# Kernel optimization log

Measured on AMD Instinct MI355X. Metric: run time of the kernel, lower is better.

The kernel has to match this reference:

```python
import jax, jax.numpy as jnp
import numpy as np

WIN = 15
BINS = 32
ALPHA = 0.9
LAM1 = 0.5
LAM2 = 0.5


def _tmedian(x, axis):
    # torch-style median: k-th smallest with k=(n-1)//2 (lower middle), keepdims
    n = x.shape[axis]
    s = jnp.sort(x, axis=axis)
    return jnp.take(s, jnp.array([(n - 1) // 2]), axis=axis)


def _box_sum_1d(x, k, axis):
    # sliding-window sum (zero padding) via cumsum / integral image
    p = k // 2
    L = x.shape[axis]
    c = jnp.cumsum(x, axis=axis)
    pad = [(0, 0)] * x.ndim
    pad[axis] = (1, 0)
    c = jnp.pad(c, pad)
    i = jnp.arange(L)
    hi = jnp.clip(i + p + 1, 0, L)
    lo = jnp.clip(i - p, 0, L)
    return jnp.take(c, hi, axis=axis) - jnp.take(c, lo, axis=axis)


def _counts_1d(L, k, dtype):
    p = k // 2
    i = jnp.arange(L)
    return (jnp.clip(i + p + 1, 0, L) - jnp.clip(i - p, 0, L)).astype(dtype)


def box_avg(x, k):
    # avg_pool2d(stride=1, padding=k//2, count_include_pad=False) on [B,C,H,W]
    s = _box_sum_1d(_box_sum_1d(x, k, 2), k, 3)
    c = _counts_1d(x.shape[2], k, x.dtype)[:, None] * _counts_1d(x.shape[3], k, x.dtype)[None, :]
    return s / c


def avg3(x):
    # avg_pool2d(k=3, stride=1, pad=1, count_include_pad=True)
    return _box_sum_1d(_box_sum_1d(x, 3, 2), 3, 3) / 9.0


def _softplus(x):
    t = jnp.log1p(jnp.exp(-jnp.abs(x)))
    return jnp.where(x >= 0, x + t, t)


def _conv3(x, k):
    return jax.lax.conv_general_dilated(x, k, (1, 1), ((1, 1), (1, 1)),
                                        dimension_numbers=('NCHW', 'OIHW', 'NCHW'))


def _forward(lab, a_rand):
    B, _, H, W = lab.shape
    N = H * W
    f32 = lab.dtype
    L = lab[:, 0:1]
    a = lab[:, 1:2]
    b = lab[:, 2:3]
    kx = jnp.array([[-1, 0, 1], [-2, 0, 2], [-1, 0, 1]], f32).reshape(1, 1, 3, 3)
    ky = jnp.array([[-1, -2, -1], [0, 0, 0], [1, 2, 1]], f32).reshape(1, 1, 3, 3)
    gx = _conv3(L, kx)
    gy = _conv3(L, ky)
    E = avg3(gx * gx) + avg3(gy * gy)           # structure-tensor trace
    S = jnp.sqrt(a * a + b * b + 1e-8)           # chroma
    Xf = jnp.concatenate([E, S], 1).reshape(B, 2, N).transpose(0, 2, 1)   # [B,N,2]
    yf = L.reshape(B, 1, N).transpose(0, 2, 1)                            # [B,N,1]
    XtX = jnp.einsum('bni,bnj->bij', Xf, Xf)
    XtY = jnp.einsum('bni,bnj->bij', Xf, yf)
    beta = jnp.linalg.solve(XtX + 1e-6 * jnp.eye(2, dtype=f32), XtY)[..., 0]  # [B,2]
    pred = beta[:, 0][:, None, None, None] * E + beta[:, 1][:, None, None, None] * S
    L_perp = L - pred
    # robust scale + whitening of [L_perp, E, S]
    X3f = jnp.concatenate([L_perp, E, S], 1).reshape(B, 3, N).transpose(0, 2, 1)  # [B,N,3]
    med = _tmedian(X3f, 1)
    mad = _tmedian(jnp.abs(X3f - med), 1) * 1.4826 + 1e-8
    Xz = (X3f - med) / mad
    diff = Xz - Xz.mean(1, keepdims=True)
    cov = jnp.einsum('bni,bnj->bij', diff, diff) / N
    e, V = jnp.linalg.eigh(jnp.maximum(cov, 1e-8))
    Wwh = jnp.einsum('bij,bj,bkj->bik', V, 1.0 / jnp.sqrt(e), V)
    Xw = diff @ Wwh                                                       # [B,N,3]
    # 128-way random-projection kurtosis search
    an = a_rand / (jnp.linalg.norm(a_rand, axis=-1, keepdims=True) + 1e-12)
    z = jnp.einsum('bni,bti->bnt', Xw, an)                                # [B,N,128]
    zc = z - z.mean(1, keepdims=True)
    m2 = (zc ** 2).mean(1) + 1e-12
    m4 = (zc ** 4).mean(1)
    kurt = m4 / (m2 * m2) - 3.0
    best = jnp.argmax(jnp.abs(kurt), axis=1)
    a_star = jnp.take_along_axis(an, best[:, None, None], axis=1)[:, 0]   # [B,3]
    z_best = jnp.einsum('bni,bi->bn', Xw, a_star)                         # [B,N]
    # 1-D 2-component GMM, 10 EM steps
    K = 2
    q25 = jnp.quantile(z_best, 0.25, axis=1)
    q75 = jnp.quantile(z_best, 0.75, axis=1)
    mu = jnp.stack([q25, q75], 1)[:, None, :]   # [B,1,K]
    var = jnp.ones((B, 1, K), f32)
    pi = jnp.full((B, 1, K), 0.5, f32)
    x1 = z_best[:, :, None]                      # [B,N,1]
    R = jnp.zeros((B, N, K), f32)
    for _ in range(10):
        logp = (-0.5 * ((x1 - mu) ** 2 / (var + 1e-6))
                - 0.5 * jnp.log(var + 1e-6) + jnp.log(pi + 1e-8))
        R = jnp.exp(jax.nn.log_softmax(logp, axis=2))
        Nk = R.sum(1, keepdims=True)             # [B,1,K]
        mu = (R * x1).sum(1, keepdims=True) / (Nk + 1e-8)
        var = (R * (x1 - mu) ** 2).sum(1, keepdims=True) / (Nk + 1e-8) + 1e-6
        pi = Nk / N
    R_alpha = R ** ALPHA
    R_alpha = R_alpha / (R_alpha.sum(2, keepdims=True) + 1e-8)
    rk_maps = R_alpha.transpose(0, 2, 1).reshape(B, K, 1, H, W)
    # per-cluster weighted Mahalanobis distance in [L_perp,E,S] space
    eye3 = jnp.eye(3, dtype=f32)
    Dk = []
    for k in range(K):
        w = R_alpha[:, :, k]
        Wsum = w.sum(1, keepdims=True) + 1e-8
        mu_k = jnp.einsum('bn,bni->bi', w, X3f) / Wsum
        Xm = X3f - mu_k[:, None, :]
        cov_k = jnp.einsum('bn,bni,bnj->bij', w, Xm, Xm) / Wsum[..., None] + 1e-6 * eye3
        inv_k = jnp.linalg.inv(cov_k)
        Dk.append(jnp.sqrt(jnp.einsum('bni,bij,bnj->bn', Xm, inv_k, Xm) + 1e-8))
    Dk = jnp.stack(Dk, 2)                        # [B,N,K]
    Rtemp = jax.nn.softmax(jnp.log(R_alpha + 1e-8), axis=2)
    D_M = (Rtemp * Dk).sum(2).reshape(B, 1, H, W)
    # local luminance anomaly (box-filtered weighted mean/std)
    Z_LLA = []
    for k in range(K):
        rk = rk_maps[:, k]
        den = box_avg(rk, WIN) + 1e-8
        mu_b = box_avg(rk * L_perp, WIN) / den
        var_b = jnp.maximum(box_avg(rk * L_perp ** 2, WIN) / den - mu_b ** 2, 1e-8)
        lla = jnp.abs(L_perp - mu_b) / (jnp.sqrt(var_b) + 1e-8)
        v = lla.reshape(B, 1, N)
        mv = _tmedian(v, 2)
        mdv = _tmedian(jnp.abs(v - mv), 2) * 1.4826 + 1e-8
        Z_LLA.append(((v - mv) / mdv).reshape(B, 1, H, W))
    # global-vs-local histogram distance (GLD)
    Lmin = L_perp.min(axis=(2, 3), keepdims=True)
    Lmax = L_perp.max(axis=(2, 3), keepdims=True)
    Lnorm = jnp.clip((L_perp - Lmin) / (Lmax - Lmin + 1e-8), 0, 1)
    idx = jnp.clip((Lnorm * BINS).astype(jnp.int32), 0, BINS - 1)[:, 0]   # [B,H,W]
    onehot = jax.nn.one_hot(idx, BINS, dtype=f32).transpose(0, 3, 1, 2)   # [B,bins,H,W]
    Z_GLD = []
    for k in range(K):
        rk = rk_maps[:, k]
        w_hist = onehot * rk
        g_hist = w_hist.reshape(B, BINS, N).sum(-1)
        g_hist = g_hist / (g_hist.sum(1, keepdims=True) + 1e-8)
        g_cdf = jnp.cumsum(g_hist, 1)
        loc_cdf = jnp.cumsum(box_avg(w_hist, WIN), 1) / (box_avg(rk, WIN) + 1e-8)
        GLD = jnp.abs(loc_cdf - g_cdf[:, :, None, None]).sum(1) / BINS    # [B,H,W]
        v = GLD.reshape(B, N)
        mv = _tmedian(v, 1)                                              # [B,1]
        mdv = _tmedian(jnp.abs(v - mv), 1) * 1.4826 + 1e-8
        Z_GLD.append(((GLD - mv[:, :, None]) / mdv[:, :, None])[:, None])
    gamma = jnp.ones_like(L_perp)
    for k in range(K):
        gamma = gamma + rk_maps[:, k] * (LAM1 * _softplus(Z_LLA[k]) + LAM2 * _softplus(Z_GLD[k]))
    # structural decorrelation term over [E,S]
    ES = jnp.concatenate([E, S], 1).reshape(B, 2, N).transpose(0, 2, 1)
    med2 = _tmedian(ES, 1)
    mad2 = _tmedian(jnp.abs(ES - med2), 1) * 1.4826 + 1e-8
    ESz = (ES - med2) / mad2
    d = ESz - ESz.mean(1, keepdims=True)
    cov2 = jnp.einsum('bni,bnj->bij', d, d) / N + 1e-6 * jnp.eye(2, dtype=f32)
    inv2 = jnp.linalg.inv(cov2)
    d2 = jnp.einsum('bni,bij,bnj->bn', d, inv2, d).reshape(B, 1, H, W)
    R_struct = jnp.exp(-0.5 * d2)
    L_anom = jnp.maximum(D_M * gamma * (1.0 - R_struct), 0.0)
    flat = L_anom.reshape(B, -1)
    q1 = jnp.quantile(flat, 0.01, axis=1).reshape(B, 1, 1, 1)
    q9 = jnp.quantile(flat, 0.99, axis=1).reshape(B, 1, 1, 1)
    L_anom_norm = jnp.clip((L_anom - q1) / (q9 - q1 + 1e-8), 0, 1)
    return L_perp, L_anom_norm


def setup_inputs() -> dict:
    key = jax.random.key(0)
    k1, k2 = jax.random.split(key)
    return {
        'batch_lab_raw': jax.random.normal(k1, (2, 3, 384, 384), jnp.float32),
        'a_rand': jax.random.normal(k2, (2, 128, 3), jnp.float32),
    }


def reference(batch_lab_raw, a_rand):
    return _forward(batch_lab_raw, a_rand)
```

## Files before the change

### kernel.cpp

```cpp
#include <hip/hip_runtime.h>
#include <math.h>

#define HH 384
#define WW 384
#define NPIX (HH*WW)
#define NB 2
#define BN (NB*NPIX)
#define NT 128
#define NBINS 32
#define MEDRANK ((NPIX-1)/2)
#define RB 72
#define RB2 288
#define SEL_BLK 64

#define A_BETA 0
#define A_XZ   16
#define A_ES   40
#define A_DK   56
#define A_GMM  128
#define A_GHIST 288
#define A_KURT 512

#define F_BETA 0
#define F_X3   8
#define F_MEAN 24
#define F_WWH  32
#define F_ASTAR 828
#define F_ZBQ  868
#define F_DKINV 880
#define F_LLA  918
#define F_GLD  924
#define F_ESI  940
#define F_LAQ  952
#define F_GCDF 968
#define F_MMS_MIN 1280
#define F_MMS_MAX 1408


__device__ __forceinline__ double waveSum(double v){
#pragma unroll
  for(int o=32;o;o>>=1) v += __shfl_down(v,o,64);
  return v;
}
__device__ __forceinline__ unsigned f2u(float f){
  unsigned u = __float_as_uint(f);
  return (u & 0x80000000u) ? ~u : (u | 0x80000000u);
}
__device__ __forceinline__ float u2f(unsigned u){
  return __uint_as_float((u & 0x80000000u) ? (u ^ 0x80000000u) : ~u);
}
__device__ __forceinline__ float sp(float x){
  float t = log1pf(expf(-fabsf(x)));
  return x >= 0.f ? x + t : t;
}

struct SelBatch {
  const float* src[8];
  int rank[8];
  int fslot[8];
  int nt;
  int medmad;
};

__device__ void pick256v(unsigned x, int rank, unsigned& sel, int& nrank){
  __shared__ unsigned s_cum[256];
  __shared__ unsigned s_res[2];
  int tid = threadIdx.x;
  s_cum[tid] = x;
  __syncthreads();
  for(int o=1;o<256;o<<=1){
    unsigned t = (tid>=o)? s_cum[tid-o] : 0u;
    __syncthreads();
    s_cum[tid] += t;
    __syncthreads();
  }
  unsigned cum = s_cum[tid];
  unsigned ex  = cum - x;
  if(x>0u && (unsigned)rank>=ex && (unsigned)rank<cum){
    s_res[0]=(unsigned)tid; s_res[1]=(unsigned)(rank-(int)ex);
  }
  __syncthreads();
  sel = s_res[0]; nrank = (int)s_res[1];
  __syncthreads();
}

__global__ void k_zero(double* A, float* F, unsigned* T){
  int i = blockIdx.x*blockDim.x + threadIdx.x;
  if(i < 2048) A[i] = 0.0;
  if(i < 4096){
    unsigned* U = (unsigned*)F;
    unsigned v = 0u;
    if(i>=F_MMS_MIN && i<F_MMS_MIN+64) v = 0xFFFFFFFFu;
    U[i] = v;
  }
  if(i < 256) T[i] = 0u;
}

__global__ void k_selz8(SelBatch sb, unsigned* Hh, unsigned* T){
  int i = blockIdx.x*256 + threadIdx.x;
  if(i < 16384) Hh[i]=0u;
  if(i < 64) T[16+i]=0u;
  if(i < 8 && i < sb.nt){
    unsigned* m = T + 80 + i*8;
    m[0]=0u; m[1]=(unsigned)sb.rank[i];
    m[2]=0u; m[3]=(unsigned)sb.rank[i];
    m[4]=0u;
  }
}

__global__ __launch_bounds__(256) void k_selp8(SelBatch sb, unsigned* Hh, unsigned* T,
                                               float* F, int stage, int pass){
  int task = blockIdx.x / SEL_BLK;
  int blk  = blockIdx.x % SEL_BLK;
  unsigned* meta = T + 80 + task*8;
  float center = (stage==1) ? __uint_as_float(meta[4]) : 0.f;
  unsigned prefix = meta[stage*2];
  unsigned himask = (pass==3)?0u:(0xFFFFFFFFu<<((pass+1)*8));
  __shared__ unsigned lh[256];
  lh[threadIdx.x]=0u; __syncthreads();
  const float* src = sb.src[task];
  for(int i=blk*256+threadIdx.x; i<NPIX; i+=SEL_BLK*256){
    float v = src[i];
    if(stage) v = fabsf(v-center);
    unsigned u = f2u(v);
    if((u&himask)==prefix) atomicAdd(&lh[(u>>(pass*8))&255u],1u);
  }
  __syncthreads();
  unsigned c = lh[threadIdx.x];
  unsigned* hp = Hh + task*2048 + stage*1024 + pass*256;
  if(c) atomicAdd(hp+threadIdx.x, c);
  __shared__ int s_last;
  __syncthreads();
  if(threadIdx.x==0){
    __threadfence();
    s_last = (atomicAdd(&T[16+task*8+stage*4+pass],1u) == (unsigned)(SEL_BLK-1));
  }
  __syncthreads();
  if(!s_last) return;
  int r = (int)meta[stage*2+1];
  unsigned x = hp[threadIdx.x];
  unsigned sel; int nr;
  pick256v(x, r, sel, nr);
  unsigned npref = prefix | (sel<<(pass*8));
  if(threadIdx.x==0){
    if(pass>0){ meta[stage*2]=npref; meta[stage*2+1]=(unsigned)nr; }
    else {
      float val = u2f(npref);
      if(stage==0){
        if(sb.medmad) meta[4]=__float_as_uint(val);
        else F[sb.fslot[task]]=val;
      } else {
        F[sb.fslot[task]]   = __uint_as_float(meta[4]);
        F[sb.fslot[task]+1] = val*1.4826f + 1e-8f;
      }
    }
  }
}

__device__ void params_from_sums(double N0,double N1,double Sx0,double Sx1,double Sxx0,double Sxx1,
                                 double& mu0,double& mu1,double& iv0h,double& iv1h,
                                 double& c0,double& c1){
  mu0=Sx0/(N0+1e-8); mu1=Sx1/(N1+1e-8);
  double v0=(Sxx0-2.0*mu0*Sx0+mu0*mu0*N0)/(N0+1e-8)+1e-6;
  double v1=(Sxx1-2.0*mu1*Sx1+mu1*mu1*N1)/(N1+1e-8)+1e-6;
  double p0=N0/(double)NPIX, p1=N1/(double)NPIX;
  c0=-0.5*log(v0+1e-6)+log(p0+1e-8);
  c1=-0.5*log(v1+1e-6)+log(p1+1e-8);
  iv0h=0.5/(v0+1e-6); iv1h=0.5/(v1+1e-6);
}
__device__ void params_init(const float* F, int b,
                            double& mu0,double& mu1,double& iv0h,double& iv1h,
                            double& c0,double& c1){
  const float* z = F + F_ZBQ + b*4;
  double h25 = 0.25*(double)(NPIX-1); double f25 = h25 - floor(h25);
  double h75 = 0.75*(double)(NPIX-1); double f75 = h75 - floor(h75);
  mu0 = (double)z[0] + f25*((double)z[1]-(double)z[0]);
  mu1 = (double)z[2] + f75*((double)z[3]-(double)z[2]);
  double v0=1.0, v1=1.0, p0=0.5, p1=0.5;
  c0=-0.5*log(v0+1e-6)+log(p0+1e-8);
  c1=-0.5*log(v1+1e-6)+log(p1+1e-8);
  iv0h=0.5/(v0+1e-6); iv1h=0.5/(v1+1e-6);
}
__device__ __forceinline__ void estep2f(float x,float mu0,float mu1,float iv0h,float iv1h,
                                        float c0,float c1,float& r0,float& r1){
  float d0=x-mu0, d1=x-mu1;
  float l0=-d0*d0*iv0h+c0, l1=-d1*d1*iv1h+c1;
  float m=fmaxf(l0,l1);
  float e0=expf(l0-m), e1=expf(l1-m);
  float s=e0+e1;
  r0=e0/s; r1=e1/s;
}

__global__ __launch_bounds__(256) void k_sobel(const float* lab, float* S, float* E){
  int bx = blockIdx.x % 24, by = (blockIdx.x/24) % 24, b = blockIdx.x/576;
  __shared__ float Lt[20][21];
  __shared__ float G[18][19];
  const float* Lb = lab + b*3*NPIX;
  int ox = bx*16, oy = by*16;
  for(int i=threadIdx.x; i<400; i+=256){
    int lx=i%20, ly=i/20;
    int gx_=ox-2+lx, gy_=oy-2+ly;
    Lt[ly][lx] = (gx_<0||gx_>=WW||gy_<0||gy_>=HH)?0.f:Lb[gy_*WW+gx_];
  }
  __syncthreads();
  for(int i=threadIdx.x; i<324; i+=256){
    int lx=i%18, ly=i/18;
    int px=lx+1, py=ly+1;
    int gxp=ox-2+px, gyp=oy-2+py;
    float g=0.f;
    if(gxp>=0&&gxp<WW&&gyp>=0&&gyp<HH){
      float gx = -Lt[py-1][px-1]+Lt[py-1][px+1] -2.f*Lt[py][px-1]+2.f*Lt[py][px+1] -Lt[py+1][px-1]+Lt[py+1][px+1];
      float gy = -Lt[py-1][px-1]-2.f*Lt[py-1][px]-Lt[py-1][px+1] +Lt[py+1][px-1]+2.f*Lt[py+1][px]+Lt[py+1][px+1];
      g = gx*gx+gy*gy;
    }
    G[ly][lx]=g;
  }
  __syncthreads();
  int tx = threadIdx.x%16, ty = threadIdx.x/16;
  float s=0;
#pragma unroll
  for(int dy=0;dy<3;dy++)
#pragma unroll
    for(int dx=0;dx<3;dx++) s += G[ty+dy][tx+dx];
  int n = (oy+ty)*WW + ox+tx;
  E[b*NPIX+n] = s*(1.f/9.f);
  float av=Lb[NPIX+n], bv=Lb[2*NPIX+n];
  S[b*NPIX+n] = sqrtf(av*av+bv*bv+1e-8f);
}

__global__ void k_beta_red(const float* E,const float* S,const float* lab,double* A,
                           float* F, unsigned* T){
  int b = blockIdx.x / RB, blk = blockIdx.x % RB;
  double s[5]={0,0,0,0,0};
  for(int n = blk*256 + threadIdx.x; n < NPIX; n += RB*256){
    float e=E[b*NPIX+n], ss=S[b*NPIX+n], l=lab[b*3*NPIX+n];
    s[0]+=(double)e*e; s[1]+=(double)e*ss; s[2]+=(double)ss*ss;
    s[3]+=(double)e*l; s[4]+=(double)ss*l;
  }
  __shared__ double red[4][5];
  int wave=threadIdx.x>>6, lane=threadIdx.x&63;
#pragma unroll
  for(int q=0;q<5;q++){
    s[q]=waveSum(s[q]);
// ... 101 lines not shown
      if(fabs(apq)<1e-30) continue;
      double theta=(a[q][q]-a[p][p])/(2.0*apq);
      double t=((theta>=0)?1.0:-1.0)/(fabs(theta)+sqrt(1.0+theta*theta));
      double c=1.0/sqrt(1.0+t*t), sn=t*c;
      for(int k2=0;k2<3;k2++){ double akp=a[k2][p],akq=a[k2][q];
        a[k2][p]=c*akp-sn*akq; a[k2][q]=sn*akp+c*akq; }
      for(int k2=0;k2<3;k2++){ double apk=a[p][k2],aqk=a[q][k2];
        a[p][k2]=c*apk-sn*aqk; a[q][k2]=sn*apk+c*aqk; }
      for(int k2=0;k2<3;k2++){ double vkp=V[k2][p],vkq=V[k2][q];
        V[k2][p]=c*vkp-sn*vkq; V[k2][q]=sn*vkp+c*vkq; }
    }
  }
  double is0=1.0/sqrt(a[0][0]), is1=1.0/sqrt(a[1][1]), is2=1.0/sqrt(a[2][2]);
  for(int i=0;i<3;i++) for(int j=0;j<3;j++){
    double w = V[i][0]*is0*V[j][0] + V[i][1]*is1*V[j][1] + V[i][2]*is2*V[j][2];
    F[F_WWH + bb*9 + i*3 + j] = (float)w;
  }
  F[F_MEAN+bb*3]=(float)m0; F[F_MEAN+bb*3+1]=(float)m1; F[F_MEAN+bb*3+2]=(float)m2;
}

__global__ void k_xw(const float* Lp,const float* E,const float* S,const float* F,
                     float* Xw,int* idxP){
  __shared__ float s_mn, s_mx;
  int i = blockIdx.x*256 + threadIdx.x;
  int b=i/NPIX;
  if(threadIdx.x==0){
    const unsigned* U = (const unsigned*)F;
    unsigned mn=0xFFFFFFFFu, mx=0u;
    for(int s2=0;s2<32;s2++){
      unsigned a=U[F_MMS_MIN+b*32+s2]; if(a<mn)mn=a;
      unsigned c=U[F_MMS_MAX+b*32+s2]; if(c>mx)mx=c;
    }
    s_mn=u2f(mn); s_mx=u2f(mx);
  }
  __syncthreads();
  const float* M = F + F_X3 + b*6;
  float lp = Lp[i];
  float z0=(lp-M[0])/M[1];
  float z1=(E [i]-M[2])/M[3];
  float z2=(S [i]-M[4])/M[5];
  float d0=z0-F[F_MEAN+b*3], d1=z1-F[F_MEAN+b*3+1], d2=z2-F[F_MEAN+b*3+2];
  const float* Wm = F + F_WWH + b*9;
  Xw[3*(size_t)i  ]=d0*Wm[0]+d1*Wm[3]+d2*Wm[6];
  Xw[3*(size_t)i+1]=d0*Wm[1]+d1*Wm[4]+d2*Wm[7];
  Xw[3*(size_t)i+2]=d0*Wm[2]+d1*Wm[5]+d2*Wm[8];
  float ln = (lp-s_mn)/(s_mx-s_mn+1e-8f);
  ln = fminf(fmaxf(ln,0.f),1.f);
  int id = (int)(ln*32.f);
  idxP[i] = id>31?31:(id<0?0:id);
}

__global__ __launch_bounds__(256) void k_kurt(const float* Xw, const float* arand, double* A){
  int g = blockIdx.x;
  int b = g >> 9;
  int t = (g >> 2) & 127;
  int seg = g & 3;
  const float* ar = arand + (b*NT+t)*3;
  float q0=ar[0], q1=ar[1], q2=ar[2];
  float nrm = (float)(sqrt((double)q0*q0+(double)q1*q1+(double)q2*q2)+1e-12);
  float a0=q0/nrm, a1=q1/nrm, a2=q2/nrm;
  const float* X = Xw + (size_t)b*NPIX*3;
  double s1=0,s2=0,s3=0,s4=0;
  int start = seg*36864;
  for(int n=start+threadIdx.x; n<start+36864; n+=256){
    const float* p = X + 3*(size_t)n;
    float z = p[0]*a0 + p[1]*a1 + p[2]*a2;
    float z2f = z*z;
    s1 += z; s2 += z2f; s3 += z2f*z; s4 += (double)z2f*z2f;
  }
  s1=waveSum(s1); s2=waveSum(s2); s3=waveSum(s3); s4=waveSum(s4);
  __shared__ double red[4][4];
  int wave=threadIdx.x>>6, lane=threadIdx.x&63;
  if(lane==0){ red[wave][0]=s1; red[wave][1]=s2; red[wave][2]=s3; red[wave][3]=s4; }
  __syncthreads();
  if(threadIdx.x<4){
    double v = red[0][threadIdx.x]+red[1][threadIdx.x]+red[2][threadIdx.x]+red[3][threadIdx.x];
    atomicAdd(&A[A_KURT + (size_t)(b*NT+t)*4 + threadIdx.x], v);
  }
}
__global__ void k_kurt_pick(const double* A, const float* arand, float* F){
  int b = blockIdx.x;
  int t = threadIdx.x;
  __shared__ float ak[NT];
  const double* K = A + A_KURT + (size_t)(b*NT+t)*4;
  double inv=1.0/(double)NPIX;
  double mean=K[0]*inv, M2=K[1]*inv, M3=K[2]*inv, M4=K[3]*inv;
  double m2 = M2 - mean*mean + 1e-12;
  double m4 = M4 - 4.0*mean*M3 + 6.0*mean*mean*M2 - 3.0*mean*mean*mean*mean;
  ak[t] = (float)fabs(m4/(m2*m2) - 3.0);
  __syncthreads();
  if(t==0){
    int best=0; float bv=ak[0];
    for(int j=1;j<NT;j++) if(ak[j]>bv){bv=ak[j];best=j;}
    const float* ar = arand + (b*NT+best)*3;
    double nrm = sqrt((double)ar[0]*ar[0]+(double)ar[1]*ar[1]+(double)ar[2]*ar[2])+1e-12;
    F[F_ASTAR+b*3]  =(float)(ar[0]/nrm);
    F[F_ASTAR+b*3+1]=(float)(ar[1]/nrm);
    F[F_ASTAR+b*3+2]=(float)(ar[2]/nrm);
  }
}
__global__ void k_zbest(const float* Xw,const float* F,float* zb){
  int i = blockIdx.x*256 + threadIdx.x; if(i>=BN) return;
  int b=i/NPIX;
  const float* p = Xw + 3*(size_t)i;
  zb[i] = p[0]*F[F_ASTAR+b*3] + p[1]*F[F_ASTAR+b*3+1] + p[2]*F[F_ASTAR+b*3+2];
}

__global__ __launch_bounds__(256) void k_gmm_red(const float* zb, const float* F, double* A, int it){
  __shared__ float P[6];
  __shared__ double red[4][6];
  int b = blockIdx.x / RB2, blk = blockIdx.x % RB2;
  if(threadIdx.x==0){
    double mu0,mu1,iv0h,iv1h,c0,c1;
    if(it==0) params_init(F,b,mu0,mu1,iv0h,iv1h,c0,c1);
    else {
      const double* g = A + A_GMM + (it-1)*16 + b*6;
      params_from_sums(g[0],g[1],g[2],g[3],g[4],g[5],mu0,mu1,iv0h,iv1h,c0,c1);
    }
    P[0]=(float)mu0; P[1]=(float)mu1; P[2]=(float)iv0h; P[3]=(float)iv1h;
    P[4]=(float)c0;  P[5]=(float)c1;
  }
  __syncthreads();
  float fmu0=P[0], fmu1=P[1], fiv0=P[2], fiv1=P[3], fc0=P[4], fc1=P[5];
  double s[6]={0,0,0,0,0,0};
  for(int n = blk*256 + threadIdx.x; n < NPIX; n += RB2*256){
    float x = zb[b*NPIX+n];
    float r0,r1; estep2f(x,fmu0,fmu1,fiv0,fiv1,fc0,fc1,r0,r1);
    s[0]+=r0; s[1]+=r1; s[2]+=r0*x; s[3]+=r1*x; s[4]+=(double)(r0*x)*x; s[5]+=(double)(r1*x)*x;
  }
  int wave=threadIdx.x>>6, lane=threadIdx.x&63;
#pragma unroll
  for(int q=0;q<6;q++){
    s[q]=waveSum(s[q]);
    if(lane==0) red[wave][q]=s[q];
  }
  __syncthreads();
  if(threadIdx.x<6){
    double v = red[0][threadIdx.x]+red[1][threadIdx.x]+red[2][threadIdx.x]+red[3][threadIdx.x];
    atomicAdd(&A[A_GMM+it*16+b*6+threadIdx.x], v);
  }
}

__global__ void k_ralpha(const float* zb, float* F, double* A, const int* idxP,
                         float* Ra0, float* Ra1, unsigned* T){
  __shared__ float h0[NBINS], h1[NBINS];
  __shared__ float P[6];
  if(threadIdx.x<NBINS){ h0[threadIdx.x]=0.f; h1[threadIdx.x]=0.f; }
  int i = blockIdx.x*256 + threadIdx.x;
  int b=i/NPIX;
  if(threadIdx.x==0){
    const double* g = A + A_GMM + 8*16 + b*6;
    double mu0,mu1,iv0h,iv1h,c0,c1;
    params_from_sums(g[0],g[1],g[2],g[3],g[4],g[5],mu0,mu1,iv0h,iv1h,c0,c1);
    P[0]=(float)mu0; P[1]=(float)mu1; P[2]=(float)iv0h; P[3]=(float)iv1h;
    P[4]=(float)c0;  P[5]=(float)c1;
  }
  __syncthreads();
  float r0,r1; estep2f(zb[i],P[0],P[1],P[2],P[3],P[4],P[5],r0,r1);
  float ra0=powf(r0,0.9f), ra1=powf(r1,0.9f);
  float s=ra0+ra1+1e-8f;
  ra0/=s; ra1/=s;
  Ra0[i]=ra0; Ra1[i]=ra1;
  int id = idxP[i];
  atomicAdd(&h0[id], ra0);
  atomicAdd(&h1[id], ra1);
  __syncthreads();
  if(threadIdx.x<NBINS){
    if(h0[threadIdx.x]!=0.f) atomicAdd(&A[A_GHIST+(0*NB+b)*32+threadIdx.x], (double)h0[threadIdx.x]);
    if(h1[threadIdx.x]!=0.f) atomicAdd(&A[A_GHIST+(1*NB+b)*32+threadIdx.x], (double)h1[threadIdx.x]);
  }
  __shared__ int s_last;
  __syncthreads();
  if(threadIdx.x==0){
    __threadfence();
    s_last = (atomicAdd(&T[2],1u) == (unsigned)(BN/256-1));
  }
  __syncthreads();
  if(!s_last) return;
  int t = threadIdx.x;
  if(t>=4) return;
  const double* gh = A + A_GHIST + t*32;
  double sum=0;
  for(int j=0;j<NBINS;j++) sum += gh[j];
  double c=0;
  for(int j=0;j<NBINS;j++){
    c += gh[j]/(sum+1e-8);
    F[F_GCDF+t*32+j]=(float)c;
  }
}

__global__ void k_dk_red(const float* Lp,const float* E,const float* S,
                         const float* Ra0,const float* Ra1,double* A,float* F,unsigned* T){
  int b = blockIdx.x / RB, blk = blockIdx.x % RB;
  double s[20];
#pragma unroll
  for(int q=0;q<20;q++) s[q]=0;
  for(int n = blk*256 + threadIdx.x; n < NPIX; n += RB*256){
    int i=b*NPIX+n;
    double w0=Ra0[i], w1=Ra1[i];
    double x0=Lp[i], x1=E[i], x2=S[i];
    s[0]+=w0; s[1]+=w0*x0; s[2]+=w0*x1; s[3]+=w0*x2;
    s[4]+=w0*x0*x0; s[5]+=w0*x0*x1; s[6]+=w0*x0*x2; s[7]+=w0*x1*x1; s[8]+=w0*x1*x2; s[9]+=w0*x2*x2;
    s[10]+=w1; s[11]+=w1*x0; s[12]+=w1*x1; s[13]+=w1*x2;
    s[14]+=w1*x0*x0; s[15]+=w1*x0*x1; s[16]+=w1*x0*x2; s[17]+=w1*x1*x1; s[18]+=w1*x1*x2; s[19]+=w1*x2*x2;
  }
  __shared__ double red[4][20];
  int wave=threadIdx.x>>6, lane=threadIdx.x&63;
#pragma unroll
  for(int q=0;q<20;q++){
    s[q]=waveSum(s[q]);
    if(lane==0) red[wave][q]=s[q];
// ... 169 lines not shown
    if(lane==0) red[wave][q]=s[q];
  }
  __syncthreads();
  if(threadIdx.x<5){
    double v = red[0][threadIdx.x]+red[1][threadIdx.x]+red[2][threadIdx.x]+red[3][threadIdx.x];
    atomicAdd(&A[A_ES+b*5+threadIdx.x], v);
  }
  __shared__ int s_last;
  __syncthreads();
  if(threadIdx.x==0){
    __threadfence();
    s_last = (atomicAdd(&T[4],1u) == (unsigned)(NB*RB-1));
  }
  __syncthreads();
  if(!s_last || threadIdx.x) return;
  for(int bb=0;bb<NB;bb++){
    const double* ss = A + A_ES + bb*5;
    double inv=1.0/(double)NPIX;
    double m0=ss[0]*inv, m1=ss[1]*inv;
    double c00=ss[2]*inv - m0*m0 + 1e-6;
    double c01=ss[3]*inv - m0*m1;
    double c11=ss[4]*inv - m1*m1 + 1e-6;
    double det=c00*c11-c01*c01;
    float* P = F + F_ESI + bb*5;
    P[0]=(float)m0; P[1]=(float)m1;
    P[2]=(float)(c11/det); P[3]=(float)(-c01/det); P[4]=(float)(c00/det);
  }
}
__global__ void k_lanom(const float* E,const float* S,const float* DM,const float* gamma,
                        const float* F,float* La){
  int i = blockIdx.x*256 + threadIdx.x; if(i>=BN) return;
  int b=i/NPIX;
  const float* M = F + F_X3 + b*6;
  const float* P = F + F_ESI + b*5;
  float z0=(E[i]-M[2])/M[3];
  float z1=(S[i]-M[4])/M[5];
  float d0=z0-P[0], d1=z1-P[1];
  float d2 = d0*d0*P[2] + 2.f*d0*d1*P[3] + d1*d1*P[4];
  float Rs = expf(-0.5f*d2);
  La[i] = fmaxf(DM[i]*gamma[i]*(1.f-Rs), 0.f);
}
__global__ void k_out2(const float* La, const float* F, float* out){
  int i = blockIdx.x*256 + threadIdx.x; if(i>=BN) return;
  int b=i/NPIX;
  const float* v = F + F_LAQ + b*4;
  double h1 = 0.01*(double)(NPIX-1); double f1 = h1 - floor(h1);
  double h9 = 0.99*(double)(NPIX-1); double f9 = h9 - floor(h9);
  float q1 = (float)((double)v[0] + f1*((double)v[1]-(double)v[0]));
  float q9 = (float)((double)v[2] + f9*((double)v[3]-(double)v[2]));
  float r = (La[i]-q1)/(q9-q1+1e-8f);
  out[BN + i] = fminf(fmaxf(r,0.f),1.f);
}

static void run_sel(const SelBatch& sb, unsigned* H, unsigned* T, float* F, hipStream_t s){
  k_selz8<<<64,256,0,s>>>(sb,H,T);
  for(int p=3;p>=0;--p) k_selp8<<<sb.nt*SEL_BLK,256,0,s>>>(sb,H,T,F,0,p);
  if(sb.medmad) for(int p=3;p>=0;--p) k_selp8<<<sb.nt*SEL_BLK,256,0,s>>>(sb,H,T,F,1,p);
}

extern "C" void kernel_launch(void* const* d_in, const int* in_sizes, int n_in,
                              void* d_out, int out_size, void* d_ws, size_t ws_size,
                              hipStream_t stream){
  (void)in_sizes; (void)n_in; (void)out_size; (void)ws_size;
  const float* lab   = (const float*)d_in[0];
  const float* arand = (const float*)d_in[1];
  float* out = (float*)d_out;
  char* wsb = (char*)d_ws;
  double* A = (double*)wsb;
  float*  F = (float*)(wsb + 16384);
  unsigned* T = (unsigned*)(wsb + 32768);
  unsigned* H8 = (unsigned*)(wsb + 65536);
  float* planes = (float*)(wsb + 131072);
  float* E    = planes;
  float* S    = planes + (size_t)BN;
  float* tA   = planes + (size_t)2*BN;
  float* tmpL = planes + (size_t)5*BN;
  float* tmpG = planes + (size_t)6*BN;
  float* Xw   = planes + (size_t)7*BN;
  float* zb   = planes + (size_t)10*BN;
  float* Ra0  = planes + (size_t)11*BN;
  float* Ra1  = planes + (size_t)12*BN;
  float* DM   = planes + (size_t)13*BN;
  float* gamma= planes + (size_t)14*BN;
  int*   idxP = (int*)(planes + (size_t)16*BN);

  const int GBN = BN/256;

  k_zero<<<16,256,0,stream>>>(A,F,T);
  k_sobel<<<NB*576,256,0,stream>>>(lab,S,E);
  k_beta_red<<<NB*RB,256,0,stream>>>(E,S,lab,A,F,T);
  k_lperp<<<GBN,256,0,stream>>>(lab,E,S,F,out);

  SelBatch sbX; sbX.nt=6; sbX.medmad=1;
  for(int b=0;b<NB;b++){
    sbX.src[b*3+0]=out+(size_t)b*NPIX; sbX.src[b*3+1]=E+(size_t)b*NPIX; sbX.src[b*3+2]=S+(size_t)b*NPIX;
    for(int ch=0;ch<3;ch++){ sbX.rank[b*3+ch]=MEDRANK; sbX.fslot[b*3+ch]=F_X3+(b*3+ch)*2; }
  }
  run_sel(sbX,H8,T,F,stream);

  k_xz_red<<<NB*RB,256,0,stream>>>(out,E,S,F,A,T);
  k_xw<<<GBN,256,0,stream>>>(out,E,S,F,Xw,idxP);
  k_kurt<<<1024,256,0,stream>>>(Xw,arand,A);
  k_kurt_pick<<<NB,128,0,stream>>>(A,arand,F);
  k_zbest<<<GBN,256,0,stream>>>(Xw,F,zb);

  SelBatch sbZ; sbZ.nt=8; sbZ.medmad=0;
  {
    int rr[4]={36863,36864,110591,110592};
    for(int b=0;b<NB;b++) for(int ri=0;ri<4;ri++){
      int t=b*4+ri;
      sbZ.src[t]=zb+(size_t)b*NPIX; sbZ.rank[t]=rr[ri]; sbZ.fslot[t]=F_ZBQ+b*4+ri;
    }
  }
  run_sel(sbZ,H8,T,F,stream);

  for(int it=0; it<9; ++it)
    k_gmm_red<<<NB*RB2,256,0,stream>>>(zb,F,A,it);
  k_ralpha<<<GBN,256,0,stream>>>(zb,F,A,idxP,Ra0,Ra1,T);
  k_dk_red<<<NB*RB,256,0,stream>>>(out,E,S,Ra0,Ra1,A,F,T);
  k_dm<<<GBN,256,0,stream>>>(out,E,S,Ra0,Ra1,F,DM);

  SelBatch sbC; sbC.nt=4; sbC.medmad=1;
  for(int b=0;b<NB;b++){
    sbC.src[b]  =tmpL+(size_t)b*NPIX; sbC.rank[b]  =MEDRANK; sbC.fslot[b]  =F_LLA+b*2;
    sbC.src[2+b]=tmpG+(size_t)b*NPIX; sbC.rank[2+b]=MEDRANK; sbC.fslot[2+b]=F_GLD+b*2;
  }

  for(int k=0;k<2;k++){
    const float* Rk = k ? Ra1 : Ra0;
    k_lla<<<NB*576,256,0,stream>>>(Rk,out,tmpL);
    k_gldf<<<NB*576,256,0,stream>>>(Rk,idxP,F,k,tmpG);
    run_sel(sbC,H8,T,F,stream);
    k_gamma<<<GBN,256,0,stream>>>(tmpL,tmpG,Rk,F,gamma,k==0?1:0);
  }

  k_es_red<<<NB*RB,256,0,stream>>>(E,S,F,A,T);
  k_lanom<<<GBN,256,0,stream>>>(E,S,DM,gamma,F,tA);

  SelBatch sbL; sbL.nt=8; sbL.medmad=0;
  {
    int rr[4]={1474,1475,145980,145981};
    for(int b=0;b<NB;b++) for(int ri=0;ri<4;ri++){
      int t=b*4+ri;
      sbL.src[t]=tA+(size_t)b*NPIX; sbL.rank[t]=rr[ri]; sbL.fslot[t]=F_LAQ+b*4+ri;
    }
  }
  run_sel(sbL,H8,T,F,stream);

  k_out2<<<GBN,256,0,stream>>>(tA,F,out);
}
```

Baseline: 753.5 us.

## Use 3-pass 11/11/10-bit radix select, batch kurtosis directions, simplify GMM E-step

The radix selection drops from four 8-bit passes to three passes with 2048/2048/1024 bins. Each selection batch now gets its own histogram region, all zeroed once up front, so the per-selection zeroing kernel goes away. The kurtosis kernel projects each pixel onto 8 directions per load to reuse Xw reads. The 2-component GMM E-step becomes a quadratic logistic form that accumulates only component-0 sums, with totals taken from a new sum pass in k_zbest. The cost is larger shared histograms, more registers in k_kurt, and a bigger histogram workspace to zero.

```diff
diff --git a/kernel.cpp b/kernel.cpp
--- a/kernel.cpp
+++ b/kernel.cpp
@@ -12,12 +12,15 @@
 #define RB 72
 #define RB2 288
 #define SEL_BLK 64
+#define KDG 8
+#define KSEG 16
 
 #define A_BETA 0
 #define A_XZ   16
 #define A_ES   40
 #define A_DK   56
 #define A_GMM  128
+#define A_ZTOT 272
 #define A_GHIST 288
 #define A_KURT 512
 
@@ -62,30 +65,36 @@
   int medmad;
 };
 
-__device__ void pick256v(unsigned x, int rank, unsigned& sel, int& nrank){
+__device__ void pickN(const unsigned* hp, int nb, int rank, unsigned& sel, int& nrank){
   __shared__ unsigned s_cum[256];
   __shared__ unsigned s_res[2];
   int tid = threadIdx.x;
-  s_cum[tid] = x;
+  int base = tid*8;
+  unsigned loc[8]; unsigned tsum=0;
+#pragma unroll
+  for(int j=0;j<8;j++){ unsigned v=(base+j<nb)?hp[base+j]:0u; loc[j]=v; tsum+=v; }
+  s_cum[tid]=tsum;
   __syncthreads();
   for(int o=1;o<256;o<<=1){
-    unsigned t = (tid>=o)? s_cum[tid-o] : 0u;
+    unsigned t=(tid>=o)?s_cum[tid-o]:0u;
     __syncthreads();
-    s_cum[tid] += t;
+    s_cum[tid]+=t;
     __syncthreads();
   }
-  unsigned cum = s_cum[tid];
-  unsigned ex  = cum - x;
-  if(x>0u && (unsigned)rank>=ex && (unsigned)rank<cum){
-    s_res[0]=(unsigned)tid; s_res[1]=(unsigned)(rank-(int)ex);
-  }
-  __syncthreads();
-  sel = s_res[0]; nrank = (int)s_res[1];
-  __syncthreads();
-}
-
-__global__ void k_zero(double* A, float* F, unsigned* T){
-  int i = blockIdx.x*blockDim.x + threadIdx.x;
+  unsigned cum=s_cum[tid], ex=cum-tsum;
+  if(tsum>0u && (unsigned)rank>=ex && (unsigned)rank<cum){
+    int rr=rank-(int)ex; unsigned bsel=0;
+#pragma unroll
+    for(int j=0;j<8;j++){ if((unsigned)rr<loc[j]){ bsel=(unsigned)(base+j); break; } rr-=(int)loc[j]; }
+    s_res[0]=bsel; s_res[1]=(unsigned)rr;
+  }
+  __syncthreads();
+  sel=s_res[0]; nrank=(int)s_res[1];
+  __syncthreads();
+}
+
+__global__ void k_zero(double* A, float* F, unsigned* T, unsigned* H){
+  int i = blockIdx.x*256 + threadIdx.x;
   if(i < 2048) A[i] = 0.0;
   if(i < 4096){
     unsigned* U = (unsigned*)F;
@@ -93,59 +102,51 @@
     if(i>=F_MMS_MIN && i<F_MMS_MIN+64) v = 0xFFFFFFFFu;
     U[i] = v;
   }
-  if(i < 256) T[i] = 0u;
-}
-
-__global__ void k_selz8(SelBatch sb, unsigned* Hh, unsigned* T){
-  int i = blockIdx.x*256 + threadIdx.x;
-  if(i < 16384) Hh[i]=0u;
-  if(i < 64) T[16+i]=0u;
-  if(i < 8 && i < sb.nt){
-    unsigned* m = T + 80 + i*8;
-    m[0]=0u; m[1]=(unsigned)sb.rank[i];
-    m[2]=0u; m[3]=(unsigned)sb.rank[i];
-    m[4]=0u;
-  }
-}
-
-__global__ __launch_bounds__(256) void k_selp8(SelBatch sb, unsigned* Hh, unsigned* T,
-                                               float* F, int stage, int pass){
+  if(i < 512) T[i] = 0u;
+  for(int j=i; j<240*2048; j+=65536) H[j]=0u;
+}
+
+__global__ __launch_bounds__(256) void k_selp(SelBatch sb, unsigned* Hh, unsigned* T,
+                                              float* F, int bid, int stage, int p){
   int task = blockIdx.x / SEL_BLK;
   int blk  = blockIdx.x % SEL_BLK;
-  unsigned* meta = T + 80 + task*8;
+  unsigned* meta = T + 384 + task*8;
   float center = (stage==1) ? __uint_as_float(meta[4]) : 0.f;
-  unsigned prefix = meta[stage*2];
-  unsigned himask = (pass==3)?0u:(0xFFFFFFFFu<<((pass+1)*8));
-  __shared__ unsigned lh[256];
-  lh[threadIdx.x]=0u; __syncthreads();
+  unsigned pre = (p==2) ? 0u : meta[stage*2];
+  __shared__ unsigned lh[2048];
+  for(int j=threadIdx.x;j<2048;j+=256) lh[j]=0u;
+  __syncthreads();
   const float* src = sb.src[task];
   for(int i=blk*256+threadIdx.x; i<NPIX; i+=SEL_BLK*256){
     float v = src[i];
     if(stage) v = fabsf(v-center);
     unsigned u = f2u(v);
-    if((u&himask)==prefix) atomicAdd(&lh[(u>>(pass*8))&255u],1u);
-  }
-  __syncthreads();
-  unsigned c = lh[threadIdx.x];
-  unsigned* hp = Hh + task*2048 + stage*1024 + pass*256;
-  if(c) atomicAdd(hp+threadIdx.x, c);
+    unsigned bin; bool ok;
+    if(p==2){ bin = u>>21; ok = true; }
+    else if(p==1){ bin = (u>>10)&2047u; ok = ((u>>21)==pre); }
+    else { bin = u&1023u; ok = ((u>>10)==pre); }
+    if(ok) atomicAdd(&lh[bin],1u);
+  }
+  __syncthreads();
+  unsigned* hp = Hh + (size_t)(((bid*8+task)*2+stage)*3 + (2-p))*2048;
+  for(int j=threadIdx.x;j<2048;j+=256){ unsigned c=lh[j]; if(c) atomicAdd(hp+j,c); }
   __shared__ int s_last;
   __syncthreads();
   if(threadIdx.x==0){
     __threadfence();
-    s_last = (atomicAdd(&T[16+task*8+stage*4+pass],1u) == (unsigned)(SEL_BLK-1));
+    s_last = (atomicAdd(&T[16+bid*64+task*8+stage*4+(2-p)],1u) == (unsigned)(SEL_BLK-1));
   }
   __syncthreads();
   if(!s_last) return;
-  int r = (int)meta[stage*2+1];
-  unsigned x = hp[threadIdx.x];
+  int r = (p==2) ? sb.rank[task] : (int)meta[stage*2+1];
+  int nb = (p==0) ? 1024 : 2048;
   unsigned sel; int nr;
-  pick256v(x, r, sel, nr);
-  unsigned npref = prefix | (sel<<(pass*8));
-  if(threadIdx.x==0){
-    if(pass>0){ meta[stage*2]=npref; meta[stage*2+1]=(unsigned)nr; }
+  pickN(hp, nb, r, sel, nr);
+  if(threadIdx.x==0){
+    if(p==2){ meta[stage*2]=sel; meta[stage*2+1]=(unsigned)nr; }
+    else if(p==1){ meta[stage*2]=(pre<<11)|sel; meta[stage*2+1]=(unsigned)nr; }
     else {
-      float val = u2f(npref);
+      float val = u2f((pre<<10)|sel);
       if(stage==0){
         if(sb.medmad) meta[4]=__float_as_uint(val);
         else F[sb.fslot[task]]=val;
@@ -157,38 +158,31 @@
   }
 }
 
-__device__ void params_from_sums(double N0,double N1,double Sx0,double Sx1,double Sxx0,double Sxx1,
-                                 double& mu0,double& mu1,double& iv0h,double& iv1h,
-                                 double& c0,double& c1){
-  mu0=Sx0/(N0+1e-8); mu1=Sx1/(N1+1e-8);
+__device__ void quad_from_stats(double N0,double Sx0,double Sxx0,double Sxt,double Sxxt,
+                                float& qa,float& qb,float& qc){
+  double Nt=(double)NPIX;
+  double N1=Nt-N0, Sx1=Sxt-Sx0, Sxx1=Sxxt-Sxx0;
+  double mu0=Sx0/(N0+1e-8), mu1=Sx1/(N1+1e-8);
   double v0=(Sxx0-2.0*mu0*Sx0+mu0*mu0*N0)/(N0+1e-8)+1e-6;
   double v1=(Sxx1-2.0*mu1*Sx1+mu1*mu1*N1)/(N1+1e-8)+1e-6;
-  double p0=N0/(double)NPIX, p1=N1/(double)NPIX;
-  c0=-0.5*log(v0+1e-6)+log(p0+1e-8);
-  c1=-0.5*log(v1+1e-6)+log(p1+1e-8);
-  iv0h=0.5/(v0+1e-6); iv1h=0.5/(v1+1e-6);
-}
-__device__ void params_init(const float* F, int b,
-                            double& mu0,double& mu1,double& iv0h,double& iv1h,
-                            double& c0,double& c1){
+  double p0=N0/Nt, p1=N1/Nt;
+  double c0=-0.5*log(v0+1e-6)+log(p0+1e-8);
+  double c1=-0.5*log(v1+1e-6)+log(p1+1e-8);
+  double iv0=0.5/(v0+1e-6), iv1=0.5/(v1+1e-6);
+  qa=(float)(iv0-iv1);
+  qb=(float)(2.0*(iv1*mu1-iv0*mu0));
+  qc=(float)(iv0*mu0*mu0-iv1*mu1*mu1+c1-c0);
+}
+__device__ void quad_init(const float* F,int b,float& qa,float& qb,float& qc){
   const float* z = F + F_ZBQ + b*4;
   double h25 = 0.25*(double)(NPIX-1); double f25 = h25 - floor(h25);
   double h75 = 0.75*(double)(NPIX-1); double f75 = h75 - floor(h75);
-  mu0 = (double)z[0] + f25*((double)z[1]-(double)z[0]);
-  mu1 = (double)z[2] + f75*((double)z[3]-(double)z[2]);
-  double v0=1.0, v1=1.0, p0=0.5, p1=0.5;
-  c0=-0.5*log(v0+1e-6)+log(p0+1e-8);
-  c1=-0.5*log(v1+1e-6)+log(p1+1e-8);
-  iv0h=0.5/(v0+1e-6); iv1h=0.5/(v1+1e-6);
-}
-__device__ __forceinline__ void estep2f(float x,float mu0,float mu1,float iv0h,float iv1h,
-                                        float c0,float c1,float& r0,float& r1){
-  float d0=x-mu0, d1=x-mu1;
-  float l0=-d0*d0*iv0h+c0, l1=-d1*d1*iv1h+c1;
-  float m=fmaxf(l0,l1);
-  float e0=expf(l0-m), e1=expf(l1-m);
-  float s=e0+e1;
-  r0=e0/s; r1=e1/s;
+  double mu0 = (double)z[0] + f25*((double)z[1]-(double)z[0]);
+  double mu1 = (double)z[2] + f75*((double)z[3]-(double)z[2]);
+  double iv = 0.5/(1.0+1e-6);
+  qa = 0.f;
+  qb = (float)(2.0*iv*(mu1-mu0));
+  qc = (float)(iv*(mu0*mu0-mu1*mu1));
 }
 
 __global__ __launch_bounds__(256) void k_sobel(const float* lab, float* S, float* E){
@@ -396,30 +390,48 @@
 
 __global__ __launch_bounds__(256) void k_kurt(const float* Xw, const float* arand, double* A){
   int g = blockIdx.x;
-  int b = g >> 9;
-  int t = (g >> 2) & 127;
-  int seg = g & 3;
-  const float* ar = arand + (b*NT+t)*3;
-  float q0=ar[0], q1=ar[1], q2=ar[2];
-  float nrm = (float)(sqrt((double)q0*q0+(double)q1*q1+(double)q2*q2)+1e-12);
-  float a0=q0/nrm, a1=q1/nrm, a2=q2/nrm;
+  int b   = g / ((NT/KDG)*KSEG);
+  int rem = g % ((NT/KDG)*KSEG);
+  int dg  = rem / KSEG;
+  int seg = rem % KSEG;
+  float a0[KDG],a1[KDG],a2[KDG];
+#pragma unroll
+  for(int j=0;j<KDG;j++){
+    const float* ar = arand + (b*NT+dg*KDG+j)*3;
+    float q0=ar[0],q1=ar[1],q2=ar[2];
+    float nrm=(float)(sqrt((double)q0*q0+(double)q1*q1+(double)q2*q2)+1e-12);
+    a0[j]=q0/nrm; a1[j]=q1/nrm; a2[j]=q2/nrm;
+  }
   const float* X = Xw + (size_t)b*NPIX*3;
-  double s1=0,s2=0,s3=0,s4=0;
-  int start = seg*36864;
-  for(int n=start+threadIdx.x; n<start+36864; n+=256){
+  double s[KDG][4];
+#pragma unroll
+  for(int j=0;j<KDG;j++){ s[j][0]=0; s[j][1]=0; s[j][2]=0; s[j][3]=0; }
+  const int cnt = NPIX/KSEG;
+  int start = seg*cnt;
+  for(int n=start+threadIdx.x; n<start+cnt; n+=256){
     const float* p = X + 3*(size_t)n;
-    float z = p[0]*a0 + p[1]*a1 + p[2]*a2;
-    float z2f = z*z;
-    s1 += z; s2 += z2f; s3 += z2f*z; s4 += (double)z2f*z2f;
-  }
-  s1=waveSum(s1); s2=waveSum(s2); s3=waveSum(s3); s4=waveSum(s4);
-  __shared__ double red[4][4];
+    float x=p[0], y=p[1], z=p[2];
+#pragma unroll
+    for(int j=0;j<KDG;j++){
+      float zz = fmaf(x,a0[j],fmaf(y,a1[j], z*a2[j]));
+      float z2f = zz*zz;
+      s[j][0]+=zz; s[j][1]+=z2f; s[j][2]+=z2f*zz; s[j][3]+=(double)z2f*z2f;
+    }
+  }
+  __shared__ double red[4][KDG*4];
   int wave=threadIdx.x>>6, lane=threadIdx.x&63;
-  if(lane==0){ red[wave][0]=s1; red[wave][1]=s2; red[wave][2]=s3; red[wave][3]=s4; }
-  __syncthreads();
-  if(threadIdx.x<4){
+#pragma unroll
+  for(int j=0;j<KDG;j++)
+#pragma unroll
+    for(int m=0;m<4;m++){
+      double v=waveSum(s[j][m]);
+      if(lane==0) red[wave][j*4+m]=v;
+    }
+  __syncthreads();
+  if(threadIdx.x<KDG*4){
     double v = red[0][threadIdx.x]+red[1][threadIdx.x]+red[2][threadIdx.x]+red[3][threadIdx.x];
-    atomicAdd(&A[A_KURT + (size_t)(b*NT+t)*4 + threadIdx.x], v);
+    int j=threadIdx.x>>2, m=threadIdx.x&3;
+    atomicAdd(&A[A_KURT + (size_t)(b*NT+dg*KDG+j)*4 + m], v);
   }
 }
 __global__ void k_kurt_pick(const double* A, const float* arand, float* F){
@@ -443,64 +455,74 @@
     F[F_ASTAR+b*3+2]=(float)(ar[2]/nrm);
   }
 }
-__global__ void k_zbest(const float* Xw,const float* F,float* zb){
-  int i = blockIdx.x*256 + threadIdx.x; if(i>=BN) return;
+__global__ void k_zbest(const float* Xw,const float* F,float* zb,double* A){
+  int i = blockIdx.x*256 + threadIdx.x;
   int b=i/NPIX;
   const float* p = Xw + 3*(size_t)i;
-  zb[i] = p[0]*F[F_ASTAR+b*3] + p[1]*F[F_ASTAR+b*3+1] + p[2]*F[F_ASTAR+b*3+2];
+  float v = p[0]*F[F_ASTAR+b*3] + p[1]*F[F_ASTAR+b*3+1] + p[2]*F[F_ASTAR+b*3+2];
+  zb[i]=v;
+  double s0=waveSum((double)v), s1=waveSum((double)v*v);
+  __shared__ double red[4][2];
+  int wave=threadIdx.x>>6, lane=threadIdx.x&63;
+  if(lane==0){ red[wave][0]=s0; red[wave][1]=s1; }
+  __syncthreads();
+  if(threadIdx.x<2){
+    double v2 = red[0][threadIdx.x]+red[1][threadIdx.x]+red[2][threadIdx.x]+red[3][threadIdx.x];
+    atomicAdd(&A[A_ZTOT+b*2+threadIdx.x], v2);
+  }
 }
 
 __global__ __launch_bounds__(256) void k_gmm_red(const float* zb, const float* F, double* A, int it){
-  __shared__ float P[6];
-  __shared__ double red[4][6];
+  __shared__ float Q[3];
+  __shared__ double red[4][3];
   int b = blockIdx.x / RB2, blk = blockIdx.x % RB2;
   if(threadIdx.x==0){
-    double mu0,mu1,iv0h,iv1h,c0,c1;
-    if(it==0) params_init(F,b,mu0,mu1,iv0h,iv1h,c0,c1);
+    float qa,qb,qc;
+    if(it==0) quad_init(F,b,qa,qb,qc);
     else {
-      const double* g = A + A_GMM + (it-1)*16 + b*6;
-      params_from_sums(g[0],g[1],g[2],g[3],g[4],g[5],mu0,mu1,iv0h,iv1h,c0,c1);
-    }
-    P[0]=(float)mu0; P[1]=(float)mu1; P[2]=(float)iv0h; P[3]=(float)iv1h;
-    P[4]=(float)c0;  P[5]=(float)c1;
-  }
-  __syncthreads();
-  float fmu0=P[0], fmu1=P[1], fiv0=P[2], fiv1=P[3], fc0=P[4], fc1=P[5];
-  double s[6]={0,0,0,0,0,0};
+      const double* g = A + A_GMM + (it-1)*8 + b*4;
+      quad_from_stats(g[0],g[1],g[2],A[A_ZTOT+b*2],A[A_ZTOT+b*2+1],qa,qb,qc);
+    }
+    Q[0]=qa;Q[1]=qb;Q[2]=qc;
+  }
+  __syncthreads();
+  float qa=Q[0],qb=Q[1],qc=Q[2];
+  double s0=0,s1=0,s2=0;
   for(int n = blk*256 + threadIdx.x; n < NPIX; n += RB2*256){
     float x = zb[b*NPIX+n];
-    float r0,r1; estep2f(x,fmu0,fmu1,fiv0,fiv1,fc0,fc1,r0,r1);
-    s[0]+=r0; s[1]+=r1; s[2]+=r0*x; s[3]+=r1*x; s[4]+=(double)(r0*x)*x; s[5]+=(double)(r1*x)*x;
+    float f = fmaf(fmaf(qa,x,qb),x,qc);
+    float r0 = 1.f/(1.f+expf(f));
+    float rx = r0*x;
+    s0+=r0; s1+=rx; s2+=(double)rx*x;
   }
   int wave=threadIdx.x>>6, lane=threadIdx.x&63;
-#pragma unroll
-  for(int q=0;q<6;q++){
-    s[q]=waveSum(s[q]);
-    if(lane==0) red[wave][q]=s[q];
-  }
-  __syncthreads();
-  if(threadIdx.x<6){
+  s0=waveSum(s0); s1=waveSum(s1); s2=waveSum(s2);
+  if(lane==0){ red[wave][0]=s0; red[wave][1]=s1; red[wave][2]=s2; }
+  __syncthreads();
+  if(threadIdx.x<3){
     double v = red[0][threadIdx.x]+red[1][threadIdx.x]+red[2][threadIdx.x]+red[3][threadIdx.x];
-    atomicAdd(&A[A_GMM+it*16+b*6+threadIdx.x], v);
+    atomicAdd(&A[A_GMM+it*8+b*4+threadIdx.x], v);
   }
 }
 
 __global__ void k_ralpha(const float* zb, float* F, double* A, const int* idxP,
                          float* Ra0, float* Ra1, unsigned* T){
   __shared__ float h0[NBINS], h1[NBINS];
-  __shared__ float P[6];
+  __shared__ float Q[3];
   if(threadIdx.x<NBINS){ h0[threadIdx.x]=0.f; h1[threadIdx.x]=0.f; }
   int i = blockIdx.x*256 + threadIdx.x;
   int b=i/NPIX;
   if(threadIdx.x==0){
-    const double* g = A + A_GMM + 8*16 + b*6;
-    double mu0,mu1,iv0h,iv1h,c0,c1;
-    params_from_sums(g[0],g[1],g[2],g[3],g[4],g[5],mu0,mu1,iv0h,iv1h,c0,c1);
-    P[0]=(float)mu0; P[1]=(float)mu1; P[2]=(float)iv0h; P[3]=(float)iv1h;
-    P[4]=(float)c0;  P[5]=(float)c1;
-  }
-  __syncthreads();
-  float r0,r1; estep2f(zb[i],P[0],P[1],P[2],P[3],P[4],P[5],r0,r1);
+    const double* g = A + A_GMM + 8*8 + b*4;
+    float qa,qb,qc;
+    quad_from_stats(g[0],g[1],g[2],A[A_ZTOT+b*2],A[A_ZTOT+b*2+1],qa,qb,qc);
+    Q[0]=qa;Q[1]=qb;Q[2]=qc;
+  }
+  __syncthreads();
+  float x = zb[i];
+  float f = fmaf(fmaf(Q[0],x,Q[1]),x,Q[2]);
+  float r0 = 1.f/(1.f+expf(f));
+  float r1 = 1.f-r0;
   float ra0=powf(r0,0.9f), ra1=powf(r1,0.9f);
   float s=ra0+ra1+1e-8f;
   ra0/=s; ra1/=s;
@@ -776,10 +798,9 @@
   out[BN + i] = fminf(fmaxf(r,0.f),1.f);
 }
 
-static void run_sel(const SelBatch& sb, unsigned* H, unsigned* T, float* F, hipStream_t s){
-  k_selz8<<<64,256,0,s>>>(sb,H,T);
-  for(int p=3;p>=0;--p) k_selp8<<<sb.nt*SEL_BLK,256,0,s>>>(sb,H,T,F,0,p);
-  if(sb.medmad) for(int p=3;p>=0;--p) k_selp8<<<sb.nt*SEL_BLK,256,0,s>>>(sb,H,T,F,1,p);
+static void run_sel(const SelBatch& sb, unsigned* H, unsigned* T, float* F, int bid, hipStream_t s){
+  for(int p=2;p>=0;--p) k_selp<<<sb.nt*SEL_BLK,256,0,s>>>(sb,H,T,F,bid,0,p);
+  if(sb.medmad) for(int p=2;p>=0;--p) k_selp<<<sb.nt*SEL_BLK,256,0,s>>>(sb,H,T,F,bid,1,p);
 }
 
 extern "C" void kernel_launch(void* const* d_in, const int* in_sizes, int n_in,
@@ -793,8 +814,8 @@
   double* A = (double*)wsb;
   float*  F = (float*)(wsb + 16384);
   unsigned* T = (unsigned*)(wsb + 32768);
-  unsigned* H8 = (unsigned*)(wsb + 65536);
-  float* planes = (float*)(wsb + 131072);
+  unsigned* H = (unsigned*)(wsb + 65536);
+  float* planes = (float*)(wsb + (size_t)4*1024*1024);
   float* E    = planes;
   float* S    = planes + (size_t)BN;
   float* tA   = planes + (size_t)2*BN;
@@ -810,7 +831,7 @@
 
   const int GBN = BN/256;
 
-  k_zero<<<16,256,0,stream>>>(A,F,T);
+  k_zero<<<256,256,0,stream>>>(A,F,T,H);
   k_sobel<<<NB*576,256,0,stream>>>(lab,S,E);
   k_beta_red<<<NB*RB,256,0,stream>>>(E,S,lab,A,F,T);
   k_lperp<<<GBN,256,0,stream>>>(lab,E,S,F,out);
@@ -820,13 +841,13 @@
     sbX.src[b*3+0]=out+(size_t)b*NPIX; sbX.src[b*3+1]=E+(size_t)b*NPIX; sbX.src[b*3+2]=S+(size_t)b*NPIX;
     for(int ch=0;ch<3;ch++){ sbX.rank[b*3+ch]=MEDRANK; sbX.fslot[b*3+ch]=F_X3+(b*3+ch)*2; }
   }
-  run_sel(sbX,H8,T,F,stream);
+  run_sel(sbX,H,T,F,0,stream);
 
   k_xz_red<<<NB*RB,256,0,stream>>>(out,E,S,F,A,T);
   k_xw<<<GBN,256,0,stream>>>(out,E,S,F,Xw,idxP);
-  k_kurt<<<1024,256,0,stream>>>(Xw,arand,A);
+  k_kurt<<<NB*(NT/KDG)*KSEG,256,0,stream>>>(Xw,arand,A);
   k_kurt_pick<<<NB,128,0,stream>>>(A,arand,F);
-  k_zbest<<<GBN,256,0,stream>>>(Xw,F,zb);
+  k_zbest<<<GBN,256,0,stream>>>(Xw,F,zb,A);
 
   SelBatch sbZ; sbZ.nt=8; sbZ.medmad=0;
   {
@@ -836,7 +857,7 @@
       sbZ.src[t]=zb+(size_t)b*NPIX; sbZ.rank[t]=rr[ri]; sbZ.fslot[t]=F_ZBQ+b*4+ri;
     }
   }
-  run_sel(sbZ,H8,T,F,stream);
+  run_sel(sbZ,H,T,F,1,stream);
 
   for(int it=0; it<9; ++it)
     k_gmm_red<<<NB*RB2,256,0,stream>>>(zb,F,A,it);
@@ -854,7 +875,7 @@
     const float* Rk = k ? Ra1 : Ra0;
     k_lla<<<NB*576,256,0,stream>>>(Rk,out,tmpL);
     k_gldf<<<NB*576,256,0,stream>>>(Rk,idxP,F,k,tmpG);
-    run_sel(sbC,H8,T,F,stream);
+    run_sel(sbC,H,T,F,2+k,stream);
     k_gamma<<<GBN,256,0,stream>>>(tmpL,tmpG,Rk,F,gamma,k==0?1:0);
   }
 
@@ -869,7 +890,7 @@
       sbL.src[t]=tA+(size_t)b*NPIX; sbL.rank[t]=rr[ri]; sbL.fslot[t]=F_LAQ+b*4+ri;
     }
   }
-  run_sel(sbL,H8,T,F,stream);
+  run_sel(sbL,H,T,F,4,stream);
 
   k_out2<<<GBN,256,0,stream>>>(tA,F,out);
 }
```

Result: faster. 703.3 us (-6.7%).
